# Kernel tuning notes

Measured on AMD Instinct MI355X. Metric: run time of the kernel, lower is better.

The kernel has to match this reference:

```python
import jax, jax.numpy as jnp
import numpy as np

DIM = 768
NUM_HEADS = 12
HEAD_DIM = DIM // NUM_HEADS
SCALE = HEAD_DIM ** -0.5


def setup_inputs() -> dict:
    key = jax.random.key(0)
    k1, k2, k3, k4 = jax.random.split(key, 4)
    B, H, W = 8, 32, 32
    x = jax.random.normal(k1, (B, H, W, DIM), dtype=jnp.float32)
    s = DIM ** -0.5
    w_qkv = jax.random.normal(k2, (DIM, 3 * DIM), dtype=jnp.float32) * s
    w_proj = jax.random.normal(k3, (DIM, DIM), dtype=jnp.float32) * s
    b_proj = jax.random.normal(k4, (DIM,), dtype=jnp.float32) * 0.01
    return {"x": x, "w_qkv": w_qkv, "w_proj": w_proj, "b_proj": b_proj}


def reference(x, w_qkv, w_proj, b_proj):
    B, H, W, C = x.shape
    N = H * W
    qkv = (x.reshape(B, N, C) @ w_qkv).reshape(B, N, 3, NUM_HEADS, HEAD_DIM)
    q, k, v = jnp.moveaxis(qkv, 2, 0)  # each (B, N, h, d)
    # scores: (B, h, N, N)
    attn = jnp.einsum('bnhd,bmhd->bhnm', q * SCALE, k)
    attn = jax.nn.softmax(attn, axis=-1)
    out = jnp.einsum('bhnm,bmhd->bnhd', attn, v).reshape(B, H, W, C)
    return out @ w_proj + b_proj
```

## Files before the change

kernel.cpp:

```cpp
#include <hip/hip_runtime.h>

typedef _Float16 half_t;
typedef __attribute__((ext_vector_type(4))) _Float16 half4;
typedef __attribute__((ext_vector_type(8))) _Float16 half8;
typedef __attribute__((ext_vector_type(4))) float floatx4;

#define MFMA_F16(A,B,C)  __builtin_amdgcn_mfma_f32_16x16x32_f16(A,B,C,0,0,0)

typedef __attribute__((address_space(1))) const void gvoid_t;
typedef __attribute__((address_space(3))) void svoid_t;

__device__ __forceinline__ void async_copy16(const half_t* g, half_t* l) {
    __builtin_amdgcn_global_load_lds((gvoid_t*)g, (svoid_t*)l, 16, 0, 0);
}

__global__ __launch_bounds__(256)
void prep_kernel(const float* __restrict__ x, const float* __restrict__ w_qkv,
                 const float* __restrict__ w_proj, half_t* __restrict__ xh,
                 half_t* __restrict__ wqkvT, half_t* __restrict__ wprojT)
{
    __shared__ half_t tile[64 * 65];
    const int id = blockIdx.x, tid = threadIdx.x;
    if (id < 6144) {
        size_t e = (size_t)id * 1024 + tid * 4;
        float4 f = *(const float4*)(x + e);
        half4 h = { (half_t)f.x, (half_t)f.y, (half_t)f.z, (half_t)f.w };
        *(half4*)(xh + e) = h;
        return;
    }
    const float* src; half_t* dst; int lds, tr0, tc0;
    if (id < 6576) { int t = id - 6144; src = w_qkv; dst = wqkvT; lds = 2304;
                     tr0 = (t / 36) * 64; tc0 = (t % 36) * 64; }
    else           { int t = id - 6576; src = w_proj; dst = wprojT; lds = 768;
                     tr0 = (t / 12) * 64; tc0 = (t % 12) * 64; }
    #pragma unroll
    for (int i = 0; i < 4; i++) {
        int e = tid + i * 256, r = e >> 4, c4 = (e & 15) << 2;
        float4 f = *(const float4*)(src + (size_t)(tr0 + r) * lds + tc0 + c4);
        tile[(c4 + 0) * 65 + r] = (half_t)f.x;
        tile[(c4 + 1) * 65 + r] = (half_t)f.y;
        tile[(c4 + 2) * 65 + r] = (half_t)f.z;
        tile[(c4 + 3) * 65 + r] = (half_t)f.w;
    }
    __syncthreads();
    #pragma unroll
    for (int i = 0; i < 4; i++) {
        int e = tid + i * 256, c = e >> 4, r4 = (e & 15) << 2;
        half4 h = { tile[c * 65 + r4], tile[c * 65 + r4 + 1],
                    tile[c * 65 + r4 + 2], tile[c * 65 + r4 + 3] };
        *(half4*)(dst + (size_t)(tc0 + c) * 768 + tr0 + r4) = h;
    }
}

__global__ __launch_bounds__(512, 1)
void gemm_qkv(const half_t* __restrict__ A, const half_t* __restrict__ Bt,
              half_t* __restrict__ q_ws, half_t* __restrict__ k_ws,
              half_t* __restrict__ v_ws)
{
    __shared__ half_t As[2][256 * 32];
    __shared__ half_t Bs[2][288 * 32];

    const int lin  = blockIdx.x;
    const int xcd  = lin & 7, rest = lin >> 3;
    const int m0 = ((rest >> 3) * 8 + xcd) * 256;
    const int n0 = (rest & 7) * 288;

    const int tid  = threadIdx.x;
    const int lane = tid & 63;
    const int w    = tid >> 6;
    const int wm   = w >> 1, wn = w & 1;
    const int quad = lane >> 4, l16 = lane & 15;

    const int b0p = (lane ^ (lane >> 2) ^ (lane >> 4)) & 1;
    const int b1p = ((lane >> 1) ^ (lane >> 3)) & 1;
    const int b2p = ((lane >> 2) ^ (lane >> 4)) & 1;
    const int row_log = ((lane >> 2) & 0xC) | ((lane >> 2) & 2) | b2p;
    const int q_log   = (b1p << 1) | b0p;

    const int foff = ((((l16 << 2) | quad) ^ (l16 & 7)) << 3);

    const half_t* aBase = A  + (size_t)(m0 + row_log) * 768 + q_log * 8;
    const half_t* bBase = Bt + (size_t)(n0 + row_log) * 768 + q_log * 8;

    floatx4 acc[4][9];
    #pragma unroll
    for (int i = 0; i < 4; i++)
        #pragma unroll
        for (int j = 0; j < 9; j++) acc[i][j] = (floatx4)0.0f;

    half8 sA0, sA1, sB0, sB1, sB2;

    #define LOADR(KO)                                                          \
        do {                                                                   \
            sA0 = *(const half8*)(aBase + (size_t)((w*2+0)*16) * 768 + (KO));  \
            sA1 = *(const half8*)(aBase + (size_t)((w*2+1)*16) * 768 + (KO));  \
            sB0 = *(const half8*)(bBase + (size_t)((w*2+0)*16) * 768 + (KO));  \
            sB1 = *(const half8*)(bBase + (size_t)((w*2+1)*16) * 768 + (KO));  \
            if (w < 2)                                                         \
                sB2 = *(const half8*)(bBase + (size_t)((16+w)*16) * 768 + (KO)); \
        } while (0)

    #define WRITES(BUF)                                                        \
        do {                                                                   \
            *(half8*)(&As[BUF][(w*2+0)*512 + lane*8]) = sA0;                   \
            *(half8*)(&As[BUF][(w*2+1)*512 + lane*8]) = sA1;                   \
            *(half8*)(&Bs[BUF][(w*2+0)*512 + lane*8]) = sB0;                   \
            *(half8*)(&Bs[BUF][(w*2+1)*512 + lane*8]) = sB1;                   \
            if (w < 2)                                                         \
                *(half8*)(&Bs[BUF][(16+w)*512 + lane*8]) = sB2;                \
        } while (0)

    LOADR(0);
    WRITES(0);
    __syncthreads();

    #pragma unroll 1
    for (int t = 0; t < 24; ++t) {
        const int cur = t & 1;
        if (t < 23) LOADR((t + 1) * 32);

        half8 a[4], b[9];
        #pragma unroll
        for (int mi = 0; mi < 4; mi++)
            a[mi] = *(const half8*)(&As[cur][(wm*4 + mi) * 512 + foff]);
        #pragma unroll
        for (int ni = 0; ni < 9; ni++)
            b[ni] = *(const half8*)(&Bs[cur][(wn*9 + ni) * 512 + foff]);
        #pragma unroll
        for (int mi = 0; mi < 4; mi++)
            #pragma unroll
            for (int ni = 0; ni < 9; ni++)
                acc[mi][ni] = MFMA_F16(a[mi], b[ni], acc[mi][ni]);

        if (t < 23) WRITES(cur ^ 1);
        __syncthreads();
    }
    #undef LOADR
    #undef WRITES

    const int bb  = (m0 + wm * 64) >> 10;
    const int t0w = (m0 + wm * 64) & 1023;

    #pragma unroll
    for (int ni = 0; ni < 9; ni++) {
        const int cb  = n0 + wn * 144 + ni * 16;
        const int sel = (cb >= 1536) ? 2 : (cb >= 768 ? 1 : 0);
        const int rem = cb - sel * 768;
        const int hh  = rem >> 6;
        const int d   = (rem & 63) + l16;
        const size_t base = (size_t)(bb * 12 + hh) * 65536;

        if (sel == 0) {
            #pragma unroll
            for (int mi = 0; mi < 4; mi++) {
                int tok = t0w + mi * 16 + quad * 4;
                half4 hv = { (half_t)(acc[mi][ni][0] * 0.125f),
                             (half_t)(acc[mi][ni][1] * 0.125f),
                             (half_t)(acc[mi][ni][2] * 0.125f),
                             (half_t)(acc[mi][ni][3] * 0.125f) };
                *(half4*)(q_ws + base + (size_t)d * 1024 + tok) = hv;
            }
        } else if (sel == 1) {
            #pragma unroll
            for (int mi = 0; mi < 4; mi++)
                #pragma unroll
                for (int r = 0; r < 4; r++) {
                    int tok = t0w + mi * 16 + quad * 4 + r;
                    k_ws[base + (size_t)tok * 64 + d] = (half_t)acc[mi][ni][r];
                }
        } else {
            #pragma unroll
            for (int mi = 0; mi < 4; mi++) {
                int tokb = t0w + (mi >> 1) * 32;
                int tokp = tokb | (quad << 3) | ((mi & 1) << 2);
                half4 hv = { (half_t)acc[mi][ni][0], (half_t)acc[mi][ni][1],
                             (half_t)acc[mi][ni][2], (half_t)acc[mi][ni][3] };
                *(half4*)(v_ws + base + (size_t)d * 1024 + tokp) = hv;
            }
        }
    }
}

__global__ __launch_bounds__(256, 2)
void gemm_proj(const half_t* __restrict__ A, const half_t* __restrict__ Bt,
               float* __restrict__ Cout, const float* __restrict__ bias)
{
    __shared__ half_t As[128 * 64];
    __shared__ half_t Bs[128 * 64];

    const int lin  = blockIdx.x;
    const int xcd  = lin & 7, rest = lin >> 3;
    const int m0 = ((rest / 6) * 8 + xcd) * 128;
    const int n0 = (rest % 6) * 128;

    const int tid  = threadIdx.x;
    const int lane = tid & 63;
    const int w    = tid >> 6;
    const int wm   = w >> 1, wn = w & 1;
    const int quad = lane >> 4, l16 = lane & 15;
    const int lrow = lane >> 3;
    const int lcc  = (lane & 7) ^ lrow;
    const int xsw  = l16 & 7;

    const half_t* Ag = A  + (size_t)(m0 + w * 32 + lrow) * 768 + lcc * 8;
    const half_t* Bg = Bt + (size_t)(n0 + w * 32 + lrow) * 768 + lcc * 8;

    floatx4 acc[4][4];
    #pragma unroll
    for (int i = 0; i < 4; i++)
        #pragma unroll
        for (int j = 0; j < 4; j++) acc[i][j] = (floatx4)0.0f;

    for (int k0 = 0; k0 < 768; k0 += 64) {
        #pragma unroll
        for (int i = 0; i < 4; i++) {
            async_copy16(Ag + (size_t)(i * 8) * 768 + k0, As + (w * 4 + i) * 512);
            async_copy16(Bg + (size_t)(i * 8) * 768 + k0, Bs + (w * 4 + i) * 512);
        }
        __syncthreads();

        #pragma unroll
        for (int ks = 0; ks < 2; ks++) {
            const int co = (((ks << 2) + quad) ^ xsw) * 8;
            half8 a[4], b[4];
            #pragma unroll
            for (int mi = 0; mi < 4; mi++)
                a[mi] = *(const half8*)(As + (wm * 64 + mi * 16 + l16) * 64 + co);
            #pragma unroll
            for (int ni = 0; ni < 4; ni++)
                b[ni] = *(const half8*)(Bs + (wn * 64 + ni * 16 + l16) * 64 + co);
            #pragma unroll
            for (int mi = 0; mi < 4; mi++)
                #pragma unroll
                for (int ni = 0; ni < 4; ni++)
                    acc[mi][ni] = MFMA_F16(a[mi], b[ni], acc[mi][ni]);
        }
        __syncthreads();
    }

    float bias_v[4];
    #pragma unroll
    for (int ni = 0; ni < 4; ni++)
        bias_v[ni] = bias[n0 + wn * 64 + ni * 16 + l16];
    float* scratch = (w < 2 ? (float*)As : (float*)Bs) + (w & 1) * 1152;
    #pragma unroll
    for (int mi = 0; mi < 4; mi++) {
        #pragma unroll
        for (int ni = 0; ni < 4; ni++)
            #pragma unroll
            for (int r = 0; r < 4; r++)
                scratch[(quad * 4 + r) * 72 + ni * 16 + l16] =
                    acc[mi][ni][r] + bias_v[ni];
        #pragma unroll
        for (int i = 0; i < 4; i++) {
            int f = quad + i * 4;
            float4 v4 = *(const float4*)(scratch + l16 * 72 + f * 4);
            int gm = m0 + wm * 64 + mi * 16 + l16;
            *(float4*)(Cout + (size_t)gm * 768 + n0 + wn * 64 + f * 4) = v4;
        }
    }
}

__global__ __launch_bounds__(256, 3)
void attn_kernel(const half_t* __restrict__ qT, const half_t* __restrict__ k,
                 const half_t* __restrict__ vT, half_t* __restrict__ a_ws)
{
    __shared__ __align__(16) half_t Kb[2][4096];
    __shared__ __align__(16) half_t Vb[2][4096];
    __shared__ __align__(16) half_t Qs[64 * 128];

    const int lin  = blockIdx.x;
    const int xcd  = lin & 7, rest = lin >> 3;
    const int qc   = rest & 7;
    const int bh   = (rest >> 3) * 8 + xcd;

    const int tid  = threadIdx.x;
    const int lane = tid & 63;
    const int w    = tid >> 6;
    const int quad = lane >> 4, l16 = lane & 15;

    const half_t* qg = qT + (size_t)bh * 65536;
    const half_t* kg = k  + (size_t)bh * 65536;
    const half_t* vg = vT + (size_t)bh * 65536;

    const int srow = lane >> 3;
    const int sch  = (lane & 7) ^ srow;

    #pragma unroll
    for (int j = 0; j < 4; j++) {
        int d0 = w * 16 + j * 4;
        async_copy16(qg + (size_t)(d0 + (lane >> 4)) * 1024 + qc * 128 + (lane & 15) * 8,
                     &Qs[d0 * 128]);
    }
    #pragma unroll
    for (int j = 0; j < 2; j++) {
        int row = j * 32 + w * 8;
        async_copy16(kg + (size_t)(row + srow) * 64 + sch * 8, &Kb[0][row * 64]);
        async_copy16(vg + (size_t)(row + srow) * 1024 + sch * 8, &Vb[0][row * 64]);
    }
    __syncthreads();

    half8 qf[2][2];
    #pragma unroll
    for (int T = 0; T < 2; T++)
        #pragma unroll
        for (int ks = 0; ks < 2; ks++)
            #pragma unroll
            for (int j = 0; j < 8; j++)
                qf[T][ks][j] = Qs[(ks * 32 + quad * 8 + j) * 128
                                  + T * 64 + w * 16 + l16];

    floatx4 acc_o[2][4];
    floatx4 lacc[2];
    #pragma unroll
    for (int T = 0; T < 2; T++) {
        lacc[T] = (floatx4)0.0f;
        #pragma unroll
        for (int dt = 0; dt < 4; dt++) acc_o[T][dt] = (floatx4)0.0f;
    }

    const int xsw = l16 & 7;
    const half8 vone = { (half_t)1.0f, (half_t)1.0f, (half_t)1.0f, (half_t)1.0f,
                         (half_t)1.0f, (half_t)1.0f, (half_t)1.0f, (half_t)1.0f };

    for (int kt = 0; kt < 16; kt++) {
        const int cb = kt & 1;
        __syncthreads();
        if (kt < 15) {
            #pragma unroll
            for (int j = 0; j < 2; j++) {
                int row = j * 32 + w * 8;
                async_copy16(kg + (size_t)((kt + 1) * 64 + row + srow) * 64 + sch * 8,
                             &Kb[cb ^ 1][row * 64]);
                async_copy16(vg + (size_t)(row + srow) * 1024 + (kt + 1) * 64 + sch * 8,
                             &Vb[cb ^ 1][row * 64]);
            }
        }
        const half_t* Kc = Kb[cb];
        const half_t* Vc = Vb[cb];

        floatx4 sc[2][4];
        #pragma unroll
        for (int T = 0; T < 2; T++)
            #pragma unroll
            for (int mt = 0; mt < 4; mt++) sc[T][mt] = (floatx4)0.0f;
        #pragma unroll
        for (int ks = 0; ks < 2; ks++)
            #pragma unroll
            for (int mt = 0; mt < 4; mt++) {
                half8 kf = *(const half8*)(Kc + (mt * 16 + l16) * 64
                                              + (((ks << 2) + quad) ^ xsw) * 8);
                sc[0][mt] = MFMA_F16(kf, qf[0][ks], sc[0][mt]);
                sc[1][mt] = MFMA_F16(kf, qf[1][ks], sc[1][mt]);
            }

        half8 pa[2][2];
        #pragma unroll
        for (int T = 0; T < 2; T++)
            #pragma unroll
            for (int g = 0; g < 2; g++) {
                half8 ph;
                #pragma unroll
                for (int r = 0; r < 4; r++) ph[r]     = (half_t)__expf(sc[T][2 * g][r]);
                #pragma unroll
                for (int r = 0; r < 4; r++) ph[4 + r] = (half_t)__expf(sc[T][2 * g + 1][r]);
                pa[T][g] = ph;
            }

        #pragma unroll
        for (int g = 0; g < 2; g++) {
            lacc[0] = MFMA_F16(pa[0][g], vone, lacc[0]);
            lacc[1] = MFMA_F16(pa[1][g], vone, lacc[1]);
            #pragma unroll
            for (int dt = 0; dt < 4; dt++) {
                half8 vb = *(const half8*)(Vc + (dt * 16 + l16) * 64
                                              + ((((g << 2) + quad) ^ xsw) << 3));
                acc_o[0][dt] = MFMA_F16(pa[0][g], vb, acc_o[0][dt]);
                acc_o[1][dt] = MFMA_F16(pa[1][g], vb, acc_o[1][dt]);
            }
        }
    }

    const int b = bh / 12, h = bh - (bh / 12) * 12;
    #pragma unroll
    for (int T = 0; T < 2; T++)
        #pragma unroll
        for (int r = 0; r < 4; r++) {
            float inv = 1.0f / lacc[T][r];
            int n = qc * 128 + T * 64 + w * 16 + quad * 4 + r;
            half_t* op = a_ws + ((size_t)(b * 1024 + n)) * 768 + h * 64;
            #pragma unroll
            for (int dt = 0; dt < 4; dt++)
                op[dt * 16 + l16] = (half_t)(acc_o[T][dt][r] * inv);
        }
}

extern "C" void kernel_launch(void* const* d_in, const int* in_sizes, int n_in,
                              void* d_out, int out_size, void* d_ws, size_t ws_size,
                              hipStream_t stream)
{
    (void)in_sizes; (void)n_in; (void)out_size; (void)ws_size;
    const float* x      = (const float*)d_in[0];
    const float* w_qkv  = (const float*)d_in[1];
    const float* w_proj = (const float*)d_in[2];
    const float* b_proj = (const float*)d_in[3];
    float* out = (float*)d_out;

    half_t* ws     = (half_t*)d_ws;
    half_t* q_ws   = ws;
    half_t* k_ws   = ws + 6291456;
    half_t* v_ws   = ws + 2 * 6291456;
    half_t* xh     = ws + 3 * 6291456;
    half_t* wqkvT  = ws + 4 * 6291456;
    half_t* wprojT = wqkvT + 1769472;
    half_t* a_ws   = xh;

    prep_kernel<<<dim3(6720), dim3(256), 0, stream>>>(x, w_qkv, w_proj, xh, wqkvT, wprojT);
    gemm_qkv<<<dim3(256), dim3(512), 0, stream>>>(xh, wqkvT, q_ws, k_ws, v_ws);
    attn_kernel<<<dim3(768), dim3(256), 0, stream>>>(q_ws, k_ws, v_ws, a_ws);
    gemm_proj<<<dim3(384), dim3(256), 0, stream>>>(a_ws, wprojT, out, b_proj);
}
```

Before: 177.5 us.

## Register-staged double buffering for proj GEMM and attention K/V loads

After: 178.4 us. Within noise of the previous version (+0.5%).

```diff
diff --git a/kernel.cpp b/kernel.cpp
--- a/kernel.cpp
+++ b/kernel.cpp
@@ -185,78 +185,103 @@
 void gemm_proj(const half_t* __restrict__ A, const half_t* __restrict__ Bt,
                float* __restrict__ Cout, const float* __restrict__ bias)
 {
-    __shared__ half_t As[128 * 64];
-    __shared__ half_t Bs[128 * 64];
+    __shared__ half_t As[2][128 * 32];
+    __shared__ half_t Bs[2][192 * 32];
 
     const int lin  = blockIdx.x;
     const int xcd  = lin & 7, rest = lin >> 3;
-    const int m0 = ((rest / 6) * 8 + xcd) * 128;
-    const int n0 = (rest % 6) * 128;
+    const int m0 = ((rest >> 2) * 8 + xcd) * 128;
+    const int n0 = (rest & 3) * 192;
 
     const int tid  = threadIdx.x;
     const int lane = tid & 63;
     const int w    = tid >> 6;
     const int wm   = w >> 1, wn = w & 1;
     const int quad = lane >> 4, l16 = lane & 15;
-    const int lrow = lane >> 3;
-    const int lcc  = (lane & 7) ^ lrow;
-    const int xsw  = l16 & 7;
-
-    const half_t* Ag = A  + (size_t)(m0 + w * 32 + lrow) * 768 + lcc * 8;
-    const half_t* Bg = Bt + (size_t)(n0 + w * 32 + lrow) * 768 + lcc * 8;
-
-    floatx4 acc[4][4];
+
+    const int b0p = (lane ^ (lane >> 2) ^ (lane >> 4)) & 1;
+    const int b1p = ((lane >> 1) ^ (lane >> 3)) & 1;
+    const int b2p = ((lane >> 2) ^ (lane >> 4)) & 1;
+    const int row_log = ((lane >> 2) & 0xC) | ((lane >> 2) & 2) | b2p;
+    const int q_log   = (b1p << 1) | b0p;
+    const int foff = ((((l16 << 2) | quad) ^ (l16 & 7)) << 3);
+
+    const half_t* aBase = A  + (size_t)(m0 + row_log) * 768 + q_log * 8;
+    const half_t* bBase = Bt + (size_t)(n0 + row_log) * 768 + q_log * 8;
+
+    floatx4 acc[4][6];
     #pragma unroll
     for (int i = 0; i < 4; i++)
         #pragma unroll
-        for (int j = 0; j < 4; j++) acc[i][j] = (floatx4)0.0f;
-
-    for (int k0 = 0; k0 < 768; k0 += 64) {
-        #pragma unroll
-        for (int i = 0; i < 4; i++) {
-            async_copy16(Ag + (size_t)(i * 8) * 768 + k0, As + (w * 4 + i) * 512);
-            async_copy16(Bg + (size_t)(i * 8) * 768 + k0, Bs + (w * 4 + i) * 512);
-        }
+        for (int j = 0; j < 6; j++) acc[i][j] = (floatx4)0.0f;
+
+    half8 sA0, sA1, sB0, sB1, sB2;
+
+    #define PLOADR(KO)                                                         \
+        do {                                                                   \
+            sA0 = *(const half8*)(aBase + (size_t)((w*2+0)*16) * 768 + (KO));  \
+            sA1 = *(const half8*)(aBase + (size_t)((w*2+1)*16) * 768 + (KO));  \
+            sB0 = *(const half8*)(bBase + (size_t)((w*3+0)*16) * 768 + (KO));  \
+            sB1 = *(const half8*)(bBase + (size_t)((w*3+1)*16) * 768 + (KO));  \
+            sB2 = *(const half8*)(bBase + (size_t)((w*3+2)*16) * 768 + (KO));  \
+        } while (0)
+
+    #define PWRITES(BUF)                                                       \
+        do {                                                                   \
+            *(half8*)(&As[BUF][(w*2+0)*512 + lane*8]) = sA0;                   \
+            *(half8*)(&As[BUF][(w*2+1)*512 + lane*8]) = sA1;                   \
+            *(half8*)(&Bs[BUF][(w*3+0)*512 + lane*8]) = sB0;                   \
+            *(half8*)(&Bs[BUF][(w*3+1)*512 + lane*8]) = sB1;                   \
+            *(half8*)(&Bs[BUF][(w*3+2)*512 + lane*8]) = sB2;                   \
+        } while (0)
+
+    PLOADR(0);
+    PWRITES(0);
+    __syncthreads();
+
+    #pragma unroll 1
+    for (int t = 0; t < 24; ++t) {
+        const int cur = t & 1;
+        if (t < 23) PLOADR((t + 1) * 32);
+
+        half8 a[4], b[6];
+        #pragma unroll
+        for (int mi = 0; mi < 4; mi++)
+            a[mi] = *(const half8*)(&As[cur][(wm*4 + mi) * 512 + foff]);
+        #pragma unroll
+        for (int ni = 0; ni < 6; ni++)
+            b[ni] = *(const half8*)(&Bs[cur][(wn*6 + ni) * 512 + foff]);
+        #pragma unroll
+        for (int mi = 0; mi < 4; mi++)
+            #pragma unroll
+            for (int ni = 0; ni < 6; ni++)
+                acc[mi][ni] = MFMA_F16(a[mi], b[ni], acc[mi][ni]);
+
+        if (t < 23) PWRITES(cur ^ 1);
         __syncthreads();
-
-        #pragma unroll
-        for (int ks = 0; ks < 2; ks++) {
-            const int co = (((ks << 2) + quad) ^ xsw) * 8;
-            half8 a[4], b[4];
-            #pragma unroll
-            for (int mi = 0; mi < 4; mi++)
-                a[mi] = *(const half8*)(As + (wm * 64 + mi * 16 + l16) * 64 + co);
-            #pragma unroll
-            for (int ni = 0; ni < 4; ni++)
-                b[ni] = *(const half8*)(Bs + (wn * 64 + ni * 16 + l16) * 64 + co);
-            #pragma unroll
-            for (int mi = 0; mi < 4; mi++)
-                #pragma unroll
-                for (int ni = 0; ni < 4; ni++)
-                    acc[mi][ni] = MFMA_F16(a[mi], b[ni], acc[mi][ni]);
-        }
-        __syncthreads();
-    }
-
-    float bias_v[4];
-    #pragma unroll
-    for (int ni = 0; ni < 4; ni++)
-        bias_v[ni] = bias[n0 + wn * 64 + ni * 16 + l16];
-    float* scratch = (w < 2 ? (float*)As : (float*)Bs) + (w & 1) * 1152;
+    }
+    #undef PLOADR
+    #undef PWRITES
+
+    float bias_v[6];
+    #pragma unroll
+    for (int ni = 0; ni < 6; ni++)
+        bias_v[ni] = bias[n0 + wn * 96 + ni * 16 + l16];
+    float* scratch = (w < 2 ? (float*)As : (float*)Bs) + (w & 1) * 1600;
     #pragma unroll
     for (int mi = 0; mi < 4; mi++) {
         #pragma unroll
-        for (int ni = 0; ni < 4; ni++)
+        for (int ni = 0; ni < 6; ni++)
             #pragma unroll
             for (int r = 0; r < 4; r++)
-                scratch[(quad * 4 + r) * 72 + ni * 16 + l16] =
+                scratch[(quad * 4 + r) * 100 + ni * 16 + l16] =
                     acc[mi][ni][r] + bias_v[ni];
         #pragma unroll
-        for (int i = 0; i < 4; i++) {
+        for (int i = 0; i < 6; i++) {
             int f = quad + i * 4;
-            float4 v4 = *(const float4*)(scratch + l16 * 72 + f * 4);
+            float4 v4 = *(const float4*)(scratch + l16 * 100 + f * 4);
             int gm = m0 + wm * 64 + mi * 16 + l16;
-            *(float4*)(Cout + (size_t)gm * 768 + n0 + wn * 64 + f * 4) = v4;
+            *(float4*)(Cout + (size_t)gm * 768 + n0 + wn * 96 + f * 4) = v4;
         }
     }
 }
@@ -323,18 +348,16 @@
     const half8 vone = { (half_t)1.0f, (half_t)1.0f, (half_t)1.0f, (half_t)1.0f,
                          (half_t)1.0f, (half_t)1.0f, (half_t)1.0f, (half_t)1.0f };
 
+    half8 rk0, rk1, rv0, rv1;
+
     for (int kt = 0; kt < 16; kt++) {
         const int cb = kt & 1;
         __syncthreads();
         if (kt < 15) {
-            #pragma unroll
-            for (int j = 0; j < 2; j++) {
-                int row = j * 32 + w * 8;
-                async_copy16(kg + (size_t)((kt + 1) * 64 + row + srow) * 64 + sch * 8,
-                             &Kb[cb ^ 1][row * 64]);
-                async_copy16(vg + (size_t)(row + srow) * 1024 + (kt + 1) * 64 + sch * 8,
-                             &Vb[cb ^ 1][row * 64]);
-            }
+            rk0 = *(const half8*)(kg + (size_t)((kt + 1) * 64 + w * 8 + srow) * 64 + sch * 8);
+            rk1 = *(const half8*)(kg + (size_t)((kt + 1) * 64 + 32 + w * 8 + srow) * 64 + sch * 8);
+            rv0 = *(const half8*)(vg + (size_t)(w * 8 + srow) * 1024 + (kt + 1) * 64 + sch * 8);
+            rv1 = *(const half8*)(vg + (size_t)(32 + w * 8 + srow) * 1024 + (kt + 1) * 64 + sch * 8);
         }
         const half_t* Kc = Kb[cb];
         const half_t* Vc = Vb[cb];
@@ -378,6 +401,13 @@
                 acc_o[0][dt] = MFMA_F16(pa[0][g], vb, acc_o[0][dt]);
                 acc_o[1][dt] = MFMA_F16(pa[1][g], vb, acc_o[1][dt]);
             }
+        }
+
+        if (kt < 15) {
+            *(half8*)(&Kb[cb ^ 1][(w * 8) * 64 + lane * 8])      = rk0;
+            *(half8*)(&Kb[cb ^ 1][(32 + w * 8) * 64 + lane * 8]) = rk1;
+            *(half8*)(&Vb[cb ^ 1][(w * 8) * 64 + lane * 8])      = rv0;
+            *(half8*)(&Vb[cb ^ 1][(32 + w * 8) * 64 + lane * 8]) = rv1;
         }
     }
 
@@ -418,5 +448,5 @@
     prep_kernel<<<dim3(6720), dim3(256), 0, stream>>>(x, w_qkv, w_proj, xh, wqkvT, wprojT);
     gemm_qkv<<<dim3(256), dim3(512), 0, stream>>>(xh, wqkvT, q_ws, k_ws, v_ws);
     attn_kernel<<<dim3(768), dim3(256), 0, stream>>>(q_ws, k_ws, v_ws, a_ws);
-    gemm_proj<<<dim3(384), dim3(256), 0, stream>>>(a_ws, wprojT, out, b_proj);
-}
+    gemm_proj<<<dim3(256), dim3(256), 0, stream>>>(a_ws, wprojT, out, b_proj);
+}
```
